# Optimization experiments

Hardware: AMD Instinct MI355X
Metric: run time of the kernel (lower is better)

Reference implementation:

```python
import jax, jax.numpy as jnp
import numpy as np

KERNEL = 3
PAD = KERNEL // 2  # 1


def setup_inputs() -> dict:
    key = jax.random.key(0)
    k1, k2, k3, k4 = jax.random.split(key, 4)
    B, C, H, W = 8, 1, 352, 1216
    affinity = jax.random.normal(k1, (B, KERNEL * KERNEL, H, W), dtype=jnp.float32)
    feature = jax.random.normal(k2, (B, C, H, W), dtype=jnp.float32)
    depth_vals = jax.random.uniform(k3, (B, C, H, W), dtype=jnp.float32, minval=0.1, maxval=80.0)
    valid = (jax.random.uniform(k4, (B, C, H, W), dtype=jnp.float32) < 0.05).astype(jnp.float32)
    sparse_depth = depth_vals * valid
    return {"affinity": affinity, "feature": feature, "sparse_depth": sparse_depth, "times": 24}


def reference(affinity, feature, sparse_depth, times):
    b, k2, h, w = affinity.shape  # k2 == 9
    aff_abs = jnp.abs(affinity)
    aff_norm = aff_abs / jnp.sum(aff_abs, axis=1, keepdims=True)  # [B,9,H,W]
    mask = jnp.sign(sparse_depth)
    feat = (1.0 - mask) * feature + mask * sparse_depth

    def step(f, _):
        fp = jnp.pad(f, ((0, 0), (0, 0), (PAD, PAD), (PAD, PAD)))
        # 9 shifted views, stacked on leading axis: [9, B, C, H, W]
        views = jnp.stack([fp[:, :, i:h + i, j:w + j]
                           for i in range(KERNEL) for j in range(KERNEL)])
        out = jnp.einsum('kbchw,bkhw->bchw', views, aff_norm)
        out = (1.0 - mask) * out + mask * sparse_depth
        return out, None

    feat, _ = jax.lax.scan(step, feat, None, length=times)
    return feat
```

## Files before the change

### kernel.cpp

```cpp
#include <hip/hip_runtime.h>

#define BATCH 8
#define HGT 352
#define WID 1216
#define HW (HGT * WID)
#define NG 304

#define KSTEP 8
#define TGX 16
#define TY  32
#define CGX 20
#define CROWS 46
#define R0GX 22
#define R0ROWS 48
#define LROW 92
#define NPAIR 10
#define PSTRIDE 48
#define NTHREADS 512
#define XTILES 19
#define YTILES 11

__global__ __launch_bounds__(256) void weights_kernel(
    const float* __restrict__ aff,
    const float* __restrict__ sparse,
    unsigned short* __restrict__ wout)
{
    const int xg = blockIdx.x * 64 + threadIdx.x;
    const int y  = blockIdx.y * 4 + threadIdx.y;
    const int b  = blockIdx.z;
    if (xg >= NG) return;
    const int x0 = xg * 4;
    const long pix = (long)y * WID + x0;
    const float* ab = aff + (long)b * 9 * HW + pix;

    float4 a[9];
    #pragma unroll
    for (int k = 0; k < 9; ++k)
        a[k] = *(const float4*)(ab + (long)k * HW);
    const float4 sp = *(const float4*)(sparse + (long)b * HW + pix);
    const float m[4] = {sp.x, sp.y, sp.z, sp.w};

    union { uint4 q[4]; unsigned short u[32]; } W;

    #pragma unroll
    for (int p = 0; p < 4; ++p) {
        float av[9], s = 0.0f;
        #pragma unroll
        for (int k = 0; k < 9; ++k) {
            const float* ap = (const float*)&a[k];
            av[k] = fabsf(ap[p]);
            s += av[k];
        }
        const float scale = 65536.0f / s;
        const bool meas = m[p] > 0.0f;
        const int korder[8] = {0, 1, 2, 3, 5, 6, 7, 8};
        #pragma unroll
        for (int ks = 0; ks < 8; ++ks) {
            float t = av[korder[ks]] * scale;
            t = fminf(t, 65535.0f);
            unsigned u = meas ? 0u : (unsigned)t;
            W.u[ks * 4 + p] = (unsigned short)u;
        }
    }

    uint4* dst = (uint4*)wout + ((long)((b * HGT + y) * NG + xg)) * 4;
    dst[0] = W.q[0]; dst[1] = W.q[1]; dst[2] = W.q[2]; dst[3] = W.q[3];
}

__device__ __forceinline__ float4 stencil_g(
    const uint4* wv4, const float* A, const float* B, const float* Cc)
{
    const unsigned* w = (const unsigned*)wv4;
    float acc[4];
    #pragma unroll
    for (int p = 0; p < 4; ++p) {
        unsigned s8 = 0; float ac = 0.0f; unsigned u;
        #define EXW(ks) ((w[((ks) * 4 + p) >> 1] >> ((p & 1) * 16)) & 0xffffu)
        u = EXW(0); s8 += u; ac += (float)u * A[p];
        u = EXW(1); s8 += u; ac += (float)u * A[p + 1];
        u = EXW(2); s8 += u; ac += (float)u * A[p + 2];
        u = EXW(3); s8 += u; ac += (float)u * B[p];
        u = EXW(4); s8 += u; ac += (float)u * B[p + 2];
        u = EXW(5); s8 += u; ac += (float)u * Cc[p];
        u = EXW(6); s8 += u; ac += (float)u * Cc[p + 1];
        u = EXW(7); s8 += u; ac += (float)u * Cc[p + 2];
        #undef EXW
        ac += (float)(65536u - s8) * B[p + 1];
        acc[p] = ac * (1.0f / 65536.0f);
    }
    return make_float4(acc[0], acc[1], acc[2], acc[3]);
}

__device__ __forceinline__ void load_win(
    const float (*fp)[LROW], int row, int px, float* V)
{
    const float* r = fp[row];
    const float4 m0 = *(const float4*)&r[px];
    const float4 m1 = *(const float4*)&r[px + 4];
    V[0] = r[px - 1];
    V[1] = m0.x; V[2] = m0.y; V[3] = m0.z; V[4] = m0.w;
    V[5] = m1.x; V[6] = m1.y; V[7] = m1.z; V[8] = m1.w;
    V[9] = r[px + 8];
}

__device__ __forceinline__ void do_step(
    const float (*fp)[LROW], float (*fq)[LROW],
    const uint4* wv0, const uint4* wv1,
    bool worker, int cy, int px)
{
    __syncthreads();
    if (worker) {
        float W0[10], W1[10], W2[10];
        load_win(fp, cy,     px, W0);
        load_win(fp, cy + 1, px, W1);
        load_win(fp, cy + 2, px, W2);
        const float4 r0 = stencil_g(wv0, W0, W1, W2);
        const float4 r1 = stencil_g(wv1, W0 + 4, W1 + 4, W2 + 4);
        *(float4*)&fq[cy + 1][px]     = r0;
        *(float4*)&fq[cy + 1][px + 4] = r1;
    }
}

__global__ __launch_bounds__(NTHREADS, 4) void prop8_kernel(
    const unsigned short* __restrict__ wgt,
    const float* __restrict__ fsrc,
    const float* __restrict__ feature,
    const float* __restrict__ sparse,
    const int first,
    float* __restrict__ fdst)
{
    __shared__ float lfA[R0ROWS][LROW];
    __shared__ float lfB[R0ROWS][LROW];

    const int tid = threadIdx.x;
    const int gx0 = blockIdx.x * TGX;
    const int y0  = blockIdx.y * TY;
    const int b   = blockIdx.z;
    const long fbase = (long)b * HW;

    for (int i = tid; i < R0GX * R0ROWS; i += NTHREADS) {
        const int rgx = i % R0GX;
        const int ry  = i / R0GX;
        const int gcx = gx0 - 3 + rgx;
        const int y   = y0 - 8 + ry;
        float4 v = make_float4(0.f, 0.f, 0.f, 0.f);
        if (gcx >= 0 && gcx < NG && y >= 0 && y < HGT) {
            const long pix = fbase + (long)y * WID + gcx * 4;
            if (first) {
                const float4 sp = *(const float4*)(sparse + pix);
                const float4 ft = *(const float4*)(feature + pix);
                v.x = sp.x > 0.f ? sp.x : ft.x;
                v.y = sp.y > 0.f ? sp.y : ft.y;
                v.z = sp.z > 0.f ? sp.z : ft.z;
                v.w = sp.w > 0.f ? sp.w : ft.w;
            } else {
                v = *(const float4*)(fsrc + pix);
            }
        }
        *(float4*)&lfA[ry][rgx * 4] = v;
    }

    const int pairx = tid / PSTRIDE;
    const int cy    = tid % PSTRIDE;
    const bool worker = (pairx < NPAIR) && (cy < CROWS);

    uint4 wv[2][4];
    #pragma unroll
    for (int g = 0; g < 2; ++g)
        #pragma unroll
        for (int j = 0; j < 4; ++j)
            wv[g][j] = make_uint4(0u, 0u, 0u, 0u);

    if (worker) {
        const int y = y0 - (KSTEP - 1) + cy;
        #pragma unroll
        for (int g = 0; g < 2; ++g) {
            const int gcx = gx0 - 2 + pairx * 2 + g;
            if (gcx >= 0 && gcx < NG && y >= 0 && y < HGT) {
                const uint4* w4 = (const uint4*)wgt + ((long)((b * HGT + y) * NG + gcx)) * 4;
                wv[g][0] = w4[0]; wv[g][1] = w4[1]; wv[g][2] = w4[2]; wv[g][3] = w4[3];
            }
        }
    }

    const int px = 8 * pairx + 4;

    do_step(lfA, lfB, wv[0], wv[1], worker, cy, px);
    #pragma unroll 1
    for (int t = 0; t < 3; ++t) {
        do_step(lfB, lfA, wv[0], wv[1], worker, cy, px);
        do_step(lfA, lfB, wv[0], wv[1], worker, cy, px);
    }

    __syncthreads();
    if (worker && pairx >= 1 && pairx <= 8 && cy >= KSTEP - 1 && cy < KSTEP - 1 + TY) {
        float W0[10], W1[10], W2[10];
        load_win(lfB, cy,     px, W0);
        load_win(lfB, cy + 1, px, W1);
        load_win(lfB, cy + 2, px, W2);
        const float4 r0 = stencil_g(wv[0], W0, W1, W2);
        const float4 r1 = stencil_g(wv[1], W0 + 4, W1 + 4, W2 + 4);
        const int y = y0 + cy - (KSTEP - 1);
        const int gcx = gx0 - 2 + pairx * 2;
        float* dp = fdst + fbase + (long)y * WID + gcx * 4;
        *(float4*)(dp)     = r0;
        *(float4*)(dp + 4) = r1;
    }
}

extern "C" void kernel_launch(void* const* d_in, const int* in_sizes, int n_in,
                              void* d_out, int out_size, void* d_ws, size_t ws_size,
                              hipStream_t stream)
{
    const float* aff     = (const float*)d_in[0];
    const float* feature = (const float*)d_in[1];
    const float* sparse  = (const float*)d_in[2];

    float* out = (float*)d_out;
    unsigned short* wgt = (unsigned short*)d_ws;
    float* imgA = (float*)((char*)d_ws + (size_t)BATCH * HGT * NG * 64);
    float* imgB = imgA + (size_t)BATCH * HW;

    {
        const dim3 blk(64, 4, 1);
        const dim3 grd((NG + 63) / 64, HGT / 4, BATCH);
        weights_kernel<<<grd, blk, 0, stream>>>(aff, sparse, wgt);
    }

    const dim3 grd(XTILES, YTILES, BATCH);
    prop8_kernel<<<grd, NTHREADS, 0, stream>>>(wgt, feature , feature, sparse, 1, imgA);
    prop8_kernel<<<grd, NTHREADS, 0, stream>>>(wgt, imgA, feature, sparse, 0, imgB);
    prop8_kernel<<<grd, NTHREADS, 0, stream>>>(wgt, imgB, feature, sparse, 0, out);
}
```

Baseline: 425.5 us.

## Remap threads pair-major and add edge-column side arrays in LDS

Threads are remapped so adjacent lanes handle adjacent column pairs of the same row instead of adjacent rows. The row stride grows to hold separate left/right halo columns, written alongside each result so window edges come from a contiguous side array. The intent is to cut LDS bank conflicts and strided scalar accesses, and occupancy is raised to 6 blocks per CU. The cost is larger shared memory per block (which may limit that occupancy), extra scalar LDS stores each step, and more register pressure.

```diff
diff --git a/kernel.cpp b/kernel.cpp
--- a/kernel.cpp
+++ b/kernel.cpp
@@ -13,9 +13,11 @@
 #define CROWS 46
 #define R0GX 22
 #define R0ROWS 48
-#define LROW 92
+#define LROW 108
+#define ELBASE 88
+#define ERBASE 98
 #define NPAIR 10
-#define PSTRIDE 48
+#define NWORK (NPAIR * CROWS)
 #define NTHREADS 512
 #define XTILES 19
 #define YTILES 11
@@ -92,36 +94,39 @@
 }
 
 __device__ __forceinline__ void load_win(
-    const float (*fp)[LROW], int row, int px, float* V)
+    const float (*fp)[LROW], int row, int px, int p, float* V)
 {
     const float* r = fp[row];
     const float4 m0 = *(const float4*)&r[px];
     const float4 m1 = *(const float4*)&r[px + 4];
-    V[0] = r[px - 1];
+    V[0] = r[ELBASE + p];
     V[1] = m0.x; V[2] = m0.y; V[3] = m0.z; V[4] = m0.w;
     V[5] = m1.x; V[6] = m1.y; V[7] = m1.z; V[8] = m1.w;
-    V[9] = r[px + 8];
+    V[9] = r[ERBASE + p];
 }
 
 __device__ __forceinline__ void do_step(
     const float (*fp)[LROW], float (*fq)[LROW],
     const uint4* wv0, const uint4* wv1,
-    bool worker, int cy, int px)
+    bool worker, int p, int cy, int px)
 {
     __syncthreads();
     if (worker) {
         float W0[10], W1[10], W2[10];
-        load_win(fp, cy,     px, W0);
-        load_win(fp, cy + 1, px, W1);
-        load_win(fp, cy + 2, px, W2);
+        load_win(fp, cy,     px, p, W0);
+        load_win(fp, cy + 1, px, p, W1);
+        load_win(fp, cy + 2, px, p, W2);
         const float4 r0 = stencil_g(wv0, W0, W1, W2);
         const float4 r1 = stencil_g(wv1, W0 + 4, W1 + 4, W2 + 4);
-        *(float4*)&fq[cy + 1][px]     = r0;
-        *(float4*)&fq[cy + 1][px + 4] = r1;
-    }
-}
-
-__global__ __launch_bounds__(NTHREADS, 4) void prop8_kernel(
+        float* q = fq[cy + 1];
+        *(float4*)&q[px]     = r0;
+        *(float4*)&q[px + 4] = r1;
+        if (p != 0) q[ERBASE + p - 1] = r0.x;
+        if (p != 9) q[ELBASE + p + 1] = r1.w;
+    }
+}
+
+__global__ __launch_bounds__(NTHREADS, 6) void prop8_kernel(
     const unsigned short* __restrict__ wgt,
     const float* __restrict__ fsrc,
     const float* __restrict__ feature,
@@ -158,11 +163,16 @@
             }
         }
         *(float4*)&lfA[ry][rgx * 4] = v;
-    }
-
-    const int pairx = tid / PSTRIDE;
-    const int cy    = tid % PSTRIDE;
-    const bool worker = (pairx < NPAIR) && (cy < CROWS);
+        if ((rgx & 1) == 0) {
+            if (rgx <= 18) lfA[ry][ELBASE + (rgx >> 1)] = v.w;
+        } else if (rgx >= 3) {
+            lfA[ry][ERBASE + ((rgx - 3) >> 1)] = v.x;
+        }
+    }
+
+    const int p  = tid % NPAIR;
+    const int r  = tid / NPAIR;
+    const bool worker = tid < NWORK;
 
     uint4 wv[2][4];
     #pragma unroll
@@ -172,10 +182,10 @@
             wv[g][j] = make_uint4(0u, 0u, 0u, 0u);
 
     if (worker) {
-        const int y = y0 - (KSTEP - 1) + cy;
+        const int y = y0 - (KSTEP - 1) + r;
         #pragma unroll
         for (int g = 0; g < 2; ++g) {
-            const int gcx = gx0 - 2 + pairx * 2 + g;
+            const int gcx = gx0 - 2 + p * 2 + g;
             if (gcx >= 0 && gcx < NG && y >= 0 && y < HGT) {
                 const uint4* w4 = (const uint4*)wgt + ((long)((b * HGT + y) * NG + gcx)) * 4;
                 wv[g][0] = w4[0]; wv[g][1] = w4[1]; wv[g][2] = w4[2]; wv[g][3] = w4[3];
@@ -183,25 +193,25 @@
         }
     }
 
-    const int px = 8 * pairx + 4;
-
-    do_step(lfA, lfB, wv[0], wv[1], worker, cy, px);
+    const int px = 8 * p + 4;
+
+    do_step(lfA, lfB, wv[0], wv[1], worker, p, r, px);
     #pragma unroll 1
     for (int t = 0; t < 3; ++t) {
-        do_step(lfB, lfA, wv[0], wv[1], worker, cy, px);
-        do_step(lfA, lfB, wv[0], wv[1], worker, cy, px);
+        do_step(lfB, lfA, wv[0], wv[1], worker, p, r, px);
+        do_step(lfA, lfB, wv[0], wv[1], worker, p, r, px);
     }
 
     __syncthreads();
-    if (worker && pairx >= 1 && pairx <= 8 && cy >= KSTEP - 1 && cy < KSTEP - 1 + TY) {
+    if (worker && p >= 1 && p <= 8 && r >= KSTEP - 1 && r < KSTEP - 1 + TY) {
         float W0[10], W1[10], W2[10];
-        load_win(lfB, cy,     px, W0);
-        load_win(lfB, cy + 1, px, W1);
-        load_win(lfB, cy + 2, px, W2);
+        load_win(lfB, r,     px, p, W0);
+        load_win(lfB, r + 1, px, p, W1);
+        load_win(lfB, r + 2, px, p, W2);
         const float4 r0 = stencil_g(wv[0], W0, W1, W2);
         const float4 r1 = stencil_g(wv[1], W0 + 4, W1 + 4, W2 + 4);
-        const int y = y0 + cy - (KSTEP - 1);
-        const int gcx = gx0 - 2 + pairx * 2;
+        const int y = y0 + r - (KSTEP - 1);
+        const int gcx = gx0 - 2 + p * 2;
         float* dp = fdst + fbase + (long)y * WID + gcx * 4;
         *(float4*)(dp)     = r0;
         *(float4*)(dp + 4) = r1;
```

After: 767.0 us. 80.3% more time.
